# Kernel optimization log

Measured on AMD Instinct MI355X. Metric: run time of the kernel, lower is better.

The kernel has to match this reference:

```python
import jax, jax.numpy as jnp
import numpy as np

B = 4096
NUM_USERS = 100000
H_DIM = 128          # HIDDEN_DIM
IN_DIM = 128 + 8 + 32  # BOARD_FEAT_DIM + ACTION_BITS + USER_EMB_DIM


def _conv(x, w, b):
    # x: [B,C,H,W], w: [O,I,3,3] (torch OIHW), padding=1 -> SAME
    y = jax.lax.conv_general_dilated(
        x, w, window_strides=(1, 1), padding='SAME',
        dimension_numbers=('NCHW', 'OIHW', 'NCHW'))
    return y + b[None, :, None, None]


def _maxpool2(x):
    return jax.lax.reduce_window(x, -jnp.inf, jax.lax.max,
                                 (1, 1, 2, 2), (1, 1, 2, 2), 'VALID')


def setup_inputs() -> dict:
    key = jax.random.key(0)
    ks = jax.random.split(key, 24)
    f32 = jnp.float32

    def n(k, shape, s=0.05):
        return jax.random.normal(k, shape, dtype=f32) * s

    return {
        'board': jax.random.uniform(ks[0], (B, 1, 32, 32), dtype=f32),
        'h': jax.random.normal(ks[1], (1, B, H_DIM), dtype=f32),
        'action_token': jax.random.randint(ks[2], (B,), 0, 256, dtype=jnp.int32),
        'user_idx': jax.random.randint(ks[3], (B,), 0, NUM_USERS, dtype=jnp.int32),
        # SmallBoardCNN params
        'conv1_w': n(ks[4], (16, 1, 3, 3)), 'conv1_b': n(ks[5], (16,)),
        'conv2_w': n(ks[6], (32, 16, 3, 3)), 'conv2_b': n(ks[7], (32,)),
        'conv3_w': n(ks[8], (64, 32, 3, 3)), 'conv3_b': n(ks[9], (64,)),
        'conv4_w': n(ks[10], (128, 64, 3, 3)), 'conv4_b': n(ks[11], (128,)),
        'proj_w': n(ks[12], (128, 128)), 'proj_b': n(ks[13], (128,)),
        # user embedding
        'emb': n(ks[14], (NUM_USERS, 32), 1.0),
        # GRU params (torch layout: [3H, in], gate order r,z,n)
        'w_ih': n(ks[15], (3 * H_DIM, IN_DIM)), 'w_hh': n(ks[16], (3 * H_DIM, H_DIM)),
        'b_ih': n(ks[17], (3 * H_DIM,)), 'b_hh': n(ks[18], (3 * H_DIM,)),
        # head
        'head_w': n(ks[19], (6, H_DIM)), 'head_b': n(ks[20], (6,)),
    }


def reference(board, h, action_token, user_idx,
              conv1_w, conv1_b, conv2_w, conv2_b, conv3_w, conv3_b,
              conv4_w, conv4_b, proj_w, proj_b, emb,
              w_ih, w_hh, b_ih, b_hh, head_w, head_b):
    # SmallBoardCNN
    x = jax.nn.relu(_conv(board, conv1_w, conv1_b))
    x = jax.nn.relu(_conv(x, conv2_w, conv2_b))
    x = _maxpool2(x)                       # [B,32,16,16]
    x = jax.nn.relu(_conv(x, conv3_w, conv3_b))
    x = _maxpool2(x)                       # [B,64,8,8]
    x = jax.nn.relu(_conv(x, conv4_w, conv4_b))
    bf = x.mean(axis=(2, 3)) @ proj_w.T + proj_b   # AdaptiveAvgPool(1,1) + Linear -> [B,128]

    # int_to_8bits, batched
    abits = ((action_token[:, None] >> jnp.arange(8)) & 1).astype(jnp.float32)  # [B,8]
    uemb = emb[user_idx]                              # [B,32]
    xin = jnp.concatenate([bf, abits, uemb], axis=1)  # [B,168]

    # single GRU step (torch GRUCell math, gate order r,z,n)
    h0 = h[0]                                         # [B,128]
    gi = xin @ w_ih.T + b_ih                          # [B,384]
    gh = h0 @ w_hh.T + b_hh
    r = jax.nn.sigmoid(gi[:, :H_DIM] + gh[:, :H_DIM])
    z = jax.nn.sigmoid(gi[:, H_DIM:2 * H_DIM] + gh[:, H_DIM:2 * H_DIM])
    n_ = jnp.tanh(gi[:, 2 * H_DIM:] + r * gh[:, 2 * H_DIM:])
    h_new = (1.0 - z) * n_ + z * h0                   # [B,128]

    logits = h_new @ head_w.T + head_b                # [B,6]
    return logits, h_new[None]                        # h_new: [1,B,128]
```

## Files before the change

kernel.cpp:

```cpp
#include <hip/hip_runtime.h>
#include <hip/hip_bf16.h>

#define BATCH 4096

typedef __attribute__((ext_vector_type(8))) short short8;
typedef __attribute__((ext_vector_type(16))) float f32x16;

#define WB1_ELEM 0
#define WB2_ELEM 512
#define WB3_ELEM 5120
#define WB4_ELEM 23552
#define WB_TOTAL 97280

#define A1_OFF 2320
#define ZS1_OFF 19728
#define A2_OFF 19792
#define ZS2_OFF 36176
#define SMEM_F 36240
#define ZS3_REL 8192
#define MEANV_OFF 8320

static __device__ __forceinline__ unsigned pack2(float a, float b) {
    __hip_bfloat16 lo = __float2bfloat16(a), hi = __float2bfloat16(b);
    unsigned short ul = *(unsigned short*)&lo, uh = *(unsigned short*)&hi;
    return ((unsigned)uh << 16) | ul;
}

static __device__ __forceinline__ void store_bf16(void* p, float v) {
    __hip_bfloat16 b = __float2bfloat16(v);
    *(unsigned short*)p = *(unsigned short*)&b;
}

__global__ void prepack_weights(const float* __restrict__ w1,
                                const float* __restrict__ w2,
                                const float* __restrict__ w3,
                                const float* __restrict__ w4,
                                __hip_bfloat16* __restrict__ wb) {
    int g = blockIdx.x * 256 + threadIdx.x;
    if (g < 512) {
        int oc = g >> 4, k = g & 15;
        float v = (oc < 16 && k < 9) ? w1[oc * 9 + k] : 0.f;
        wb[g] = __float2bfloat16(v);
    } else if (g < WB3_ELEM) {
        int gg = g - WB2_ELEM;
        int oc = gg / 144, r = gg - oc * 144, tap = r >> 4, ic = r & 15;
        wb[g] = __float2bfloat16(w2[oc * 144 + ic * 9 + tap]);
    } else if (g < WB4_ELEM) {
        int gg = g - WB3_ELEM;
        int oc = gg / 288, r = gg - oc * 288, tap = r >> 5, ic = r & 31;
        wb[g] = __float2bfloat16(w3[oc * 288 + ic * 9 + tap]);
    } else if (g < WB_TOTAL) {
        int gg = g - WB4_ELEM;
        int oc = gg / 576, r = gg - oc * 576, tap = r >> 6, ic = r & 63;
        wb[g] = __float2bfloat16(w4[oc * 576 + ic * 9 + tap]);
    }
}

__global__ __launch_bounds__(256, 4) void cnn_fused_kernel(
    const float* __restrict__ board,
    const float* __restrict__ b1, const float* __restrict__ b2,
    const float* __restrict__ b3, const float* __restrict__ b4,
    const float* __restrict__ pw, const float* __restrict__ pb,
    const __hip_bfloat16* __restrict__ wb,
    float* __restrict__ bf_out)
{
    __shared__ alignas(16) char smem[SMEM_F];
    unsigned short* sbu = (unsigned short*)smem;
    char* a1b = smem + A1_OFF;
    char* a3b = smem;
    float* meanv = (float*)(smem + MEANV_OFF);

    const int t = threadIdx.x;
    const int img = blockIdx.x;
    const int w = t >> 6;
    const int l = t & 63;
    const int n = l & 31;
    const int h = l >> 5;

    const char* wb3 = (const char*)(wb + WB3_ELEM);
    const char* wb4 = (const char*)(wb + WB4_ELEM);

    {
        if (t < 132) {
            int i = t, row, col;
            if (i < 34)       { row = 0;  col = i; }
            else if (i < 68)  { row = 33; col = i - 34; }
            else if (i < 100) { row = i - 68 + 1;  col = 0; }
            else              { row = i - 100 + 1; col = 33; }
            sbu[row * 34 + col] = 0;
        }
        uint4 z; z.x = z.y = z.z = z.w = 0u;
        if (t >= 136 && t < 140) ((uint4*)(smem + ZS1_OFF))[t - 136] = z;
        else if (t >= 140 && t < 144) ((uint4*)(smem + ZS2_OFF))[t - 140] = z;
    }
    __syncthreads();

    {
        float4 v = ((const float4*)board)[img * 256 + t];
        const int p0 = t * 4;
        const int row = (p0 >> 5) + 1, col = (p0 & 31) + 1;
        unsigned short* d = sbu + row * 34 + col;
        __hip_bfloat16 x0 = __float2bfloat16(v.x), x1 = __float2bfloat16(v.y);
        __hip_bfloat16 x2 = __float2bfloat16(v.z), x3 = __float2bfloat16(v.w);
        d[0] = *(unsigned short*)&x0; d[1] = *(unsigned short*)&x1;
        d[2] = *(unsigned short*)&x2; d[3] = *(unsigned short*)&x3;
    }
    __syncthreads();

#pragma unroll 1
    for (int band = 0; band < 2; ++band) {
        const int base = band * 15;

        {
            const short8 A1 = *(const short8*)((const char*)wb + (n * 16 + h * 8) * 2);
            float b1s[8];
#pragma unroll
            for (int r = 0; r < 8; ++r) b1s[r] = b1[(r & 3) + 8 * (r >> 2) + 4 * h];
            const unsigned* sbw = (const unsigned*)smem;
#pragma unroll 1
            for (int yi = 0; yi < 5; ++yi) {
                if (yi == 4 && w != 0) break;
                const int yg = (yi < 4) ? (base + 4 * w + yi) : (base + 16);
                unsigned short c[3][3];
#pragma unroll
                for (int dy = 0; dy < 3; ++dy) {
                    const int sbase = (yg + dy) * 17 + (n >> 1);
                    const unsigned w0 = sbw[sbase], w1v = sbw[sbase + 1];
                    if (n & 1) {
                        c[dy][0] = (unsigned short)(w0 >> 16);
                        c[dy][1] = (unsigned short)(w1v & 0xffff);
                        c[dy][2] = (unsigned short)(w1v >> 16);
                    } else {
                        c[dy][0] = (unsigned short)(w0 & 0xffff);
                        c[dy][1] = (unsigned short)(w0 >> 16);
                        c[dy][2] = (unsigned short)(w1v & 0xffff);
                    }
                }
                short8 Bv;
                if (h == 0) {
                    Bv[0] = (short)c[0][0]; Bv[1] = (short)c[0][1]; Bv[2] = (short)c[0][2];
                    Bv[3] = (short)c[1][0]; Bv[4] = (short)c[1][1]; Bv[5] = (short)c[1][2];
                    Bv[6] = (short)c[2][0]; Bv[7] = (short)c[2][1];
                } else {
                    Bv = (short8)0;
                    Bv[0] = (short)c[2][2];
                }
                f32x16 acc = __builtin_amdgcn_mfma_f32_32x32x16_bf16(A1, Bv, (f32x16)0.0f, 0, 0, 0);
                float v8[8];
#pragma unroll
                for (int r = 0; r < 8; ++r) v8[r] = fmaxf(acc[r] + b1s[r], 0.f);
                const int key = ((n >> 2) & 1) << 4;
                char* dst = a1b + ((yg - base) * 32 + n) * 32;
                uint2 u0, u1;
                u0.x = pack2(v8[0], v8[1]); u0.y = pack2(v8[2], v8[3]);
                u1.x = pack2(v8[4], v8[5]); u1.y = pack2(v8[6], v8[7]);
                *(uint2*)(dst + ((h * 8) ^ key)) = u0;
                *(uint2*)(dst + ((h * 8 + 16) ^ key)) = u1;
            }
        }
        __syncthreads();

        {
            const char* wb2 = (const char*)(wb + WB2_ELEM);
            short8 Bw[9];
#pragma unroll
            for (int tp = 0; tp < 9; ++tp)
                Bw[tp] = *(const short8*)(wb2 + (n * 144 + tp * 16 + h * 8) * 2);
            const float biasv = b2[n];
            const int y_off = 2 * ((n >> 2) & 1) + ((n >> 1) & 1);
            const int x_off = 2 * ((n >> 3) & 3) + (n & 1);
            const int py_base = 8 * band + 2 * w;
            const int yb = 16 * band + 4 * w + y_off;

#pragma unroll 1
            for (int pxh = 0; pxh < 2; ++pxh) {
                const int x0 = 16 * pxh + x_off;
                f32x16 acc0 = (f32x16)0.0f, acc1 = (f32x16)0.0f;
#pragma unroll
                for (int tp = 0; tp < 9; ++tp) {
                    const int dy = tp / 3, dx = tp - 3 * dy;
                    const int lr = yb + dy - 1 - base;
                    const int c0 = x0 + dx - 1, c1 = x0 + 8 + dx - 1;
                    const bool okr = (unsigned)lr < 17u;
                    const int off0 = (okr && (unsigned)c0 < 32u)
                        ? (A1_OFF + (lr * 32 + c0) * 32 + ((h * 16) ^ (((c0 >> 2) & 1) << 4)))
                        : (ZS1_OFF + h * 16);
                    const int off1 = (okr && (unsigned)c1 < 32u)
                        ? (A1_OFF + (lr * 32 + c1) * 32 + ((h * 16) ^ (((c1 >> 2) & 1) << 4)))
                        : (ZS1_OFF + h * 16);
                    short8 A0 = *(const short8*)(smem + off0);
                    short8 A1v = *(const short8*)(smem + off1);
                    acc0 = __builtin_amdgcn_mfma_f32_32x32x16_bf16(A0, Bw[tp], acc0, 0, 0, 0);
                    acc1 = __builtin_amdgcn_mfma_f32_32x32x16_bf16(A1v, Bw[tp], acc1, 0, 0, 0);
                }
                const int py = py_base + h;
#pragma unroll
                for (int e = 0; e < 2; ++e) {
                    const f32x16 acc = e ? acc1 : acc0;
                    const int pxb = 2 * pxh + e;
#pragma unroll
                    for (int j = 0; j < 4; ++j) {
                        float v = fmaxf(fmaxf(acc[4 * j], acc[4 * j + 1]),
                                        fmaxf(acc[4 * j + 2], acc[4 * j + 3]));
                        v = fmaxf(v + biasv, 0.f);
                        const int px = 4 * pxb + j;
                        const int key = (py + 2 * px) & 3;
                        store_bf16(smem + A2_OFF + (py * 16 + px) * 64 +
                                   ((((n >> 3) ^ key) & 3) << 4) + ((n * 2) & 15), v);
                    }
                }
            }
        }
        __syncthreads();
    }

    {
        uint4 z; z.x = z.y = z.z = z.w = 0u;
        if (t < 8) ((uint4*)(a3b + ZS3_REL))[t] = z;
    }
    __syncthreads();

    {
        const int y_off = 2 * ((n >> 2) & 1) + ((n >> 1) & 1);
        const int x_off = 2 * ((n >> 3) & 3) + (n & 1);
        const int y_in = 4 * w + y_off;
        f32x16 acc00 = (f32x16)0.0f, acc01 = (f32x16)0.0f;
        f32x16 acc10 = (f32x16)0.0f, acc11 = (f32x16)0.0f;
#pragma unroll
        for (int step = 0; step < 18; ++step) {
            const int tp = step >> 1, kh = step & 1;
            const int dy = tp / 3, dx = tp - 3 * dy;
            short8 B0 = *(const short8*)(wb3 + ((n)      * 288 + tp * 32 + kh * 16 + h * 8) * 2);
            short8 B1 = *(const short8*)(wb3 + ((32 + n) * 288 + tp * 32 + kh * 16 + h * 8) * 2);
            const int row_u = y_in + dy - 1;
            const int col0 = x_off + dx - 1;
            const int col1 = col0 + 8;
            const int sbase = kh * 32 + h * 16;
            const bool okr = (unsigned)row_u < 16u;
            const int off0 = (okr && (unsigned)col0 < 16u)
                ? (A2_OFF + row_u * 1024 + col0 * 64 + (sbase ^ (((row_u + 2 * col0) & 3) << 4)))
                : (ZS2_OFF + sbase);
            const int off1 = (okr && (unsigned)col1 < 16u)
                ? (A2_OFF + row_u * 1024 + col1 * 64 + (sbase ^ (((row_u + 2 * col1) & 3) << 4)))
                : (ZS2_OFF + sbase);
            short8 A0 = *(const short8*)(smem + off0);
            short8 A1v = *(const short8*)(smem + off1);
            acc00 = __builtin_amdgcn_mfma_f32_32x32x16_bf16(A0, B0, acc00, 0, 0, 0);
            acc01 = __builtin_amdgcn_mfma_f32_32x32x16_bf16(A0, B1, acc01, 0, 0, 0);
            acc10 = __builtin_amdgcn_mfma_f32_32x32x16_bf16(A1v, B0, acc10, 0, 0, 0);
            acc11 = __builtin_amdgcn_mfma_f32_32x32x16_bf16(A1v, B1, acc11, 0, 0, 0);
        }
        const int py = 2 * w + h;
#pragma unroll
        for (int e = 0; e < 4; ++e) {
            const f32x16 acc = (e == 0) ? acc00 : (e == 1) ? acc01 : (e == 2) ? acc10 : acc11;
            const int pxb = e >> 1, ocb = e & 1;
            const float biasv = b3[32 * ocb + n];
#pragma unroll
            for (int j = 0; j < 4; ++j) {
                float v = fmaxf(fmaxf(acc[4 * j], acc[4 * j + 1]),
                                fmaxf(acc[4 * j + 2], acc[4 * j + 3]));
                v = fmaxf(v + biasv, 0.f);
                const int px = 4 * pxb + j;
                const int byte_in = ocb * 64 + n * 2;
                const int key3 = (py + 2 * px) & 7;
                store_bf16(a3b + (py * 8 + px) * 128 +
                           ((((byte_in >> 4) ^ key3) << 4) | (byte_in & 15)), v);
            }
        }
    }
    __syncthreads();

    {
        const int x4 = n & 7, y4 = (n >> 3) & 3;
        f32x16 aE0 = (f32x16)0.0f, aO0 = (f32x16)0.0f;
        f32x16 aE1 = (f32x16)0.0f, aO1 = (f32x16)0.0f;
#pragma unroll
        for (int dy = 0; dy < 3; ++dy)
#pragma unroll
            for (int dx = 0; dx < 3; ++dx) {
                const int row0 = y4 + dy - 1;
                const int col_u = x4 + dx - 1;
                const bool okc = (unsigned)col_u < 8u;
                const bool ok0 = okc && ((unsigned)row0 < 8u);
                const bool ok1 = okc && ((unsigned)(row0 + 4) < 8u);
#pragma unroll
                for (int kc = 0; kc < 4; ++kc) {
                    const int s4 = kc * 32 + h * 16;
                    const int off0 = ok0
                        ? ((row0 * 8 + col_u) * 128 + (s4 ^ (((row0 + 2 * col_u) & 7) << 4)))
                        : (ZS3_REL + s4);
                    const int off1 = ok1
                        ? (((row0 + 4) * 8 + col_u) * 128 + (s4 ^ (((row0 + 4 + 2 * col_u) & 7) << 4)))
                        : (ZS3_REL + s4);
                    short8 B = *(const short8*)(wb4 + ((32 * w + n) * 576 + (dy * 3 + dx) * 64 + kc * 16 + h * 8) * 2);
                    short8 A0 = *(const short8*)(a3b + off0);
                    short8 A1v = *(const short8*)(a3b + off1);
                    if (kc & 1) {
                        aO0 = __builtin_amdgcn_mfma_f32_32x32x16_bf16(A0, B, aO0, 0, 0, 0);
                        aO1 = __builtin_amdgcn_mfma_f32_32x32x16_bf16(A1v, B, aO1, 0, 0, 0);
                    } else {
                        aE0 = __builtin_amdgcn_mfma_f32_32x32x16_bf16(A0, B, aE0, 0, 0, 0);
                        aE1 = __builtin_amdgcn_mfma_f32_32x32x16_bf16(A1v, B, aE1, 0, 0, 0);
                    }
                }
            }
        const float biasv = b4[32 * w + n];
        float s = 0.f;
#pragma unroll
        for (int r = 0; r < 16; ++r) {
            s += fmaxf(aE0[r] + aO0[r] + biasv, 0.f);
            s += fmaxf(aE1[r] + aO1[r] + biasv, 0.f);
        }
        s += __shfl_xor(s, 32);
        if (l < 32) meanv[32 * w + l] = s * (1.f / 64.f);
    }
    __syncthreads();

    {
        const int o = t >> 1, kh = t & 1;
        const float* wrow = pw + o * 128 + kh * 64;
        const float* mv = meanv + kh * 64;
        float acc = 0.f;
        for (int k = 0; k < 64; ++k) acc = fmaf(mv[k], wrow[k], acc);
        acc += __shfl_xor(acc, 1);
        if (kh == 0) bf_out[img * 128 + o] = acc + pb[o];
    }
}

__global__ __launch_bounds__(384) void gru_kernel(
    const float* __restrict__ hin,
    const int* __restrict__ atok, const int* __restrict__ uidx,
    const float* __restrict__ emb,
    const float* __restrict__ w_ih, const float* __restrict__ w_hh,
    const float* __restrict__ b_ih, const float* __restrict__ b_hh,
    const float* __restrict__ head_w, const float* __restrict__ head_b,
    float* __restrict__ out)
{
    const int img0 = blockIdx.x * 8;
    const int t = threadIdx.x;
    __shared__ float xin_s[8][176];
    __shared__ float h0_s[8][128];
    __shared__ float gis[8][384];
    __shared__ float ghs[8][384];
    __shared__ float hn_s[8][128];
    const float* bf = out + BATCH * 6;

    for (int idx = t; idx < 8 * 176; idx += 384) {
        const int r = idx / 176, k = idx - r * 176;
        const int row = img0 + r;
        float v;
        if (k < 128)      v = bf[row * 128 + k];
        else if (k < 136) v = (float)((atok[row] >> (k - 128)) & 1);
        else if (k < 168) v = emb[uidx[row] * 32 + (k - 136)];
        else              v = 0.f;
        xin_s[r][k] = v;
    }
    for (int idx = t; idx < 8 * 128; idx += 384) {
        const int r = idx >> 7, k = idx & 127;
        h0_s[r][k] = hin[(img0 + r) * 128 + k];
    }
    __syncthreads();

    {
        const int o = t;
        float gi[8], gh[8];
        const float bi = b_ih[o], bh = b_hh[o];
#pragma unroll
        for (int r = 0; r < 8; ++r) { gi[r] = bi; gh[r] = bh; }
        const float* wi = w_ih + o * 168;
        const float* wh = w_hh + o * 128;
#pragma unroll 2
        for (int k = 0; k < 168; k += 4) {
            const float4 wv = *(const float4*)(wi + k);
#pragma unroll
            for (int r = 0; r < 8; ++r) {
                const float4 xv = *(const float4*)(&xin_s[r][k]);
                float a = fmaf(wv.x, xv.x, gi[r]);
                a = fmaf(wv.y, xv.y, a);
                a = fmaf(wv.z, xv.z, a);
                gi[r] = fmaf(wv.w, xv.w, a);
            }
        }
#pragma unroll 2
        for (int k = 0; k < 128; k += 4) {
            const float4 wv = *(const float4*)(wh + k);
#pragma unroll
            for (int r = 0; r < 8; ++r) {
                const float4 xv = *(const float4*)(&h0_s[r][k]);
                float a = fmaf(wv.x, xv.x, gh[r]);
                a = fmaf(wv.y, xv.y, a);
                a = fmaf(wv.z, xv.z, a);
                gh[r] = fmaf(wv.w, xv.w, a);
            }
        }
#pragma unroll
        for (int r = 0; r < 8; ++r) { gis[r][o] = gi[r]; ghs[r][o] = gh[r]; }
    }
    __syncthreads();

    if (t < 128) {
#pragma unroll
        for (int r = 0; r < 8; ++r) {
            const float rg = 1.f / (1.f + expf(-(gis[r][t] + ghs[r][t])));
            const float z  = 1.f / (1.f + expf(-(gis[r][128 + t] + ghs[r][128 + t])));
            const float nn = tanhf(gis[r][256 + t] + rg * ghs[r][256 + t]);
            const float hn = (1.f - z) * nn + z * h0_s[r][t];
            hn_s[r][t] = hn;
            out[BATCH * 6 + (img0 + r) * 128 + t] = hn;
        }
    }
    __syncthreads();

    if (t < 48) {
        const int r = t / 6, j = t - r * 6;
        float acc = head_b[j];
        const float* wrow = head_w + j * 128;
        for (int k = 0; k < 128; ++k) acc = fmaf(hn_s[r][k], wrow[k], acc);
        out[(img0 + r) * 6 + j] = acc;
    }
}

extern "C" void kernel_launch(void* const* d_in, const int* in_sizes, int n_in,
                              void* d_out, int out_size, void* d_ws, size_t ws_size,
                              hipStream_t stream) {
    const float* board = (const float*)d_in[0];
    const float* h     = (const float*)d_in[1];
    const int*   atok  = (const int*)d_in[2];
    const int*   uidx  = (const int*)d_in[3];
    const float* w1 = (const float*)d_in[4];
    const float* b1 = (const float*)d_in[5];
    const float* w2 = (const float*)d_in[6];
    const float* b2 = (const float*)d_in[7];
    const float* w3 = (const float*)d_in[8];
    const float* b3 = (const float*)d_in[9];
    const float* w4 = (const float*)d_in[10];
    const float* b4 = (const float*)d_in[11];
    const float* pw = (const float*)d_in[12];
    const float* pb = (const float*)d_in[13];
    const float* emb  = (const float*)d_in[14];
    const float* w_ih = (const float*)d_in[15];
    const float* w_hh = (const float*)d_in[16];
    const float* b_ih = (const float*)d_in[17];
    const float* b_hh = (const float*)d_in[18];
    const float* head_w = (const float*)d_in[19];
    const float* head_b = (const float*)d_in[20];
    float* out = (float*)d_out;
    __hip_bfloat16* wb = (__hip_bfloat16*)d_ws;

    float* bf = out + BATCH * 6;
    prepack_weights<<<(WB_TOTAL + 255) / 256, 256, 0, stream>>>(w1, w2, w3, w4, wb);
    cnn_fused_kernel<<<BATCH, 256, 0, stream>>>(board, b1, b2, b3, b4,
                                                pw, pb, wb, bf);
    gru_kernel<<<BATCH / 8, 384, 0, stream>>>(h, atok, uidx, emb, w_ih, w_hh,
                                              b_ih, b_hh, head_w, head_b, out);
}
```

Measured before the change: 191.8 us.

## Fuse GRU step and head into the per-image CNN kernel

Moves the GRU cell and output head into the CNN kernel so each block computes the features, gates and logits for its own image in shared memory. This drops the second kernel launch and the global write/read of the board features. In exchange, the GRU and head weights are streamed once per image instead of once per 8 images, which loses register reuse across rows and raises L2 traffic.

```diff
diff --git a/kernel.cpp b/kernel.cpp
--- a/kernel.cpp
+++ b/kernel.cpp
@@ -19,6 +19,11 @@
 #define SMEM_F 36240
 #define ZS3_REL 8192
 #define MEANV_OFF 8320
+#define GXIN_OFF 8832
+#define GH0_OFF 9536
+#define GGI_OFF 10048
+#define GGH_OFF 11584
+#define GHN_OFF 13120
 
 static __device__ __forceinline__ unsigned pack2(float a, float b) {
     __hip_bfloat16 lo = __float2bfloat16(a), hi = __float2bfloat16(b);
@@ -58,17 +63,28 @@
 
 __global__ __launch_bounds__(256, 4) void cnn_fused_kernel(
     const float* __restrict__ board,
+    const float* __restrict__ hin,
+    const int* __restrict__ atok, const int* __restrict__ uidx,
+    const float* __restrict__ emb,
     const float* __restrict__ b1, const float* __restrict__ b2,
     const float* __restrict__ b3, const float* __restrict__ b4,
     const float* __restrict__ pw, const float* __restrict__ pb,
+    const float* __restrict__ w_ih, const float* __restrict__ w_hh,
+    const float* __restrict__ b_ih, const float* __restrict__ b_hh,
+    const float* __restrict__ head_w, const float* __restrict__ head_b,
     const __hip_bfloat16* __restrict__ wb,
-    float* __restrict__ bf_out)
+    float* __restrict__ out)
 {
     __shared__ alignas(16) char smem[SMEM_F];
     unsigned short* sbu = (unsigned short*)smem;
     char* a1b = smem + A1_OFF;
     char* a3b = smem;
     float* meanv = (float*)(smem + MEANV_OFF);
+    float* xin = (float*)(smem + GXIN_OFF);
+    float* h0v = (float*)(smem + GH0_OFF);
+    float* gis = (float*)(smem + GGI_OFF);
+    float* ghs = (float*)(smem + GGH_OFF);
+    float* hnv = (float*)(smem + GHN_OFF);
 
     const int t = threadIdx.x;
     const int img = blockIdx.x;
@@ -217,6 +233,16 @@
     {
         uint4 z; z.x = z.y = z.z = z.w = 0u;
         if (t < 8) ((uint4*)(a3b + ZS3_REL))[t] = z;
+        else if (t >= 8 && t < 136) {
+            const int k = t - 8;
+            h0v[k] = hin[(size_t)img * 128 + k];
+        } else if (t < 144) {
+            const int k = t - 136 + 128;
+            xin[k] = (float)((atok[img] >> (k - 128)) & 1);
+        } else if (t < 176) {
+            const int k = t - 144 + 136;
+            xin[k] = emb[(size_t)uidx[img] * 32 + (k - 136)];
+        }
     }
     __syncthreads();
 
@@ -324,100 +350,61 @@
         float acc = 0.f;
         for (int k = 0; k < 64; ++k) acc = fmaf(mv[k], wrow[k], acc);
         acc += __shfl_xor(acc, 1);
-        if (kh == 0) bf_out[img * 128 + o] = acc + pb[o];
-    }
-}
-
-__global__ __launch_bounds__(384) void gru_kernel(
-    const float* __restrict__ hin,
-    const int* __restrict__ atok, const int* __restrict__ uidx,
-    const float* __restrict__ emb,
-    const float* __restrict__ w_ih, const float* __restrict__ w_hh,
-    const float* __restrict__ b_ih, const float* __restrict__ b_hh,
-    const float* __restrict__ head_w, const float* __restrict__ head_b,
-    float* __restrict__ out)
-{
-    const int img0 = blockIdx.x * 8;
-    const int t = threadIdx.x;
-    __shared__ float xin_s[8][176];
-    __shared__ float h0_s[8][128];
-    __shared__ float gis[8][384];
-    __shared__ float ghs[8][384];
-    __shared__ float hn_s[8][128];
-    const float* bf = out + BATCH * 6;
-
-    for (int idx = t; idx < 8 * 176; idx += 384) {
-        const int r = idx / 176, k = idx - r * 176;
-        const int row = img0 + r;
-        float v;
-        if (k < 128)      v = bf[row * 128 + k];
-        else if (k < 136) v = (float)((atok[row] >> (k - 128)) & 1);
-        else if (k < 168) v = emb[uidx[row] * 32 + (k - 136)];
-        else              v = 0.f;
-        xin_s[r][k] = v;
-    }
-    for (int idx = t; idx < 8 * 128; idx += 384) {
-        const int r = idx >> 7, k = idx & 127;
-        h0_s[r][k] = hin[(img0 + r) * 128 + k];
-    }
-    __syncthreads();
-
-    {
-        const int o = t;
-        float gi[8], gh[8];
-        const float bi = b_ih[o], bh = b_hh[o];
-#pragma unroll
-        for (int r = 0; r < 8; ++r) { gi[r] = bi; gh[r] = bh; }
-        const float* wi = w_ih + o * 168;
-        const float* wh = w_hh + o * 128;
+        if (kh == 0) xin[o] = acc + pb[o];
+    }
+    __syncthreads();
+
+    {
+#pragma unroll 1
+        for (int o = t; o < 384; o += 256) {
+            float gi = b_ih[o], gh = b_hh[o];
+            const float* wi = w_ih + o * 168;
+            const float* wh = w_hh + o * 128;
 #pragma unroll 2
-        for (int k = 0; k < 168; k += 4) {
-            const float4 wv = *(const float4*)(wi + k);
-#pragma unroll
-            for (int r = 0; r < 8; ++r) {
-                const float4 xv = *(const float4*)(&xin_s[r][k]);
-                float a = fmaf(wv.x, xv.x, gi[r]);
+            for (int k = 0; k < 168; k += 4) {
+                const float4 wv = *(const float4*)(wi + k);
+                const float4 xv = *(const float4*)(xin + k);
+                float a = fmaf(wv.x, xv.x, gi);
                 a = fmaf(wv.y, xv.y, a);
                 a = fmaf(wv.z, xv.z, a);
-                gi[r] = fmaf(wv.w, xv.w, a);
-            }
-        }
+                gi = fmaf(wv.w, xv.w, a);
+            }
 #pragma unroll 2
-        for (int k = 0; k < 128; k += 4) {
-            const float4 wv = *(const float4*)(wh + k);
-#pragma unroll
-            for (int r = 0; r < 8; ++r) {
-                const float4 xv = *(const float4*)(&h0_s[r][k]);
-                float a = fmaf(wv.x, xv.x, gh[r]);
+            for (int k = 0; k < 128; k += 4) {
+                const float4 wv = *(const float4*)(wh + k);
+                const float4 xv = *(const float4*)(h0v + k);
+                float a = fmaf(wv.x, xv.x, gh);
                 a = fmaf(wv.y, xv.y, a);
                 a = fmaf(wv.z, xv.z, a);
-                gh[r] = fmaf(wv.w, xv.w, a);
-            }
-        }
-#pragma unroll
-        for (int r = 0; r < 8; ++r) { gis[r][o] = gi[r]; ghs[r][o] = gh[r]; }
+                gh = fmaf(wv.w, xv.w, a);
+            }
+            gis[o] = gi;
+            ghs[o] = gh;
+        }
     }
     __syncthreads();
 
     if (t < 128) {
-#pragma unroll
-        for (int r = 0; r < 8; ++r) {
-            const float rg = 1.f / (1.f + expf(-(gis[r][t] + ghs[r][t])));
-            const float z  = 1.f / (1.f + expf(-(gis[r][128 + t] + ghs[r][128 + t])));
-            const float nn = tanhf(gis[r][256 + t] + rg * ghs[r][256 + t]);
-            const float hn = (1.f - z) * nn + z * h0_s[r][t];
-            hn_s[r][t] = hn;
-            out[BATCH * 6 + (img0 + r) * 128 + t] = hn;
-        }
-    }
-    __syncthreads();
-
-    if (t < 48) {
-        const int r = t / 6, j = t - r * 6;
-        float acc = head_b[j];
-        const float* wrow = head_w + j * 128;
-        for (int k = 0; k < 128; ++k) acc = fmaf(hn_s[r][k], wrow[k], acc);
-        out[(img0 + r) * 6 + j] = acc;
+        const float rg = 1.f / (1.f + expf(-(gis[t] + ghs[t])));
+        const float zz = 1.f / (1.f + expf(-(gis[128 + t] + ghs[128 + t])));
+        const float nn = tanhf(gis[256 + t] + rg * ghs[256 + t]);
+        const float hn = (1.f - zz) * nn + zz * h0v[t];
+        hnv[t] = hn;
+        out[BATCH * 6 + (size_t)img * 128 + t] = hn;
+    }
+    __syncthreads();
+
+    if (t < 192) {
+        const int j = t >> 5, lane = t & 31;
+        const float4 wv = *(const float4*)(head_w + j * 128 + lane * 4);
+        const float4 hv = *(const float4*)(hnv + lane * 4);
+        float s = wv.x * hv.x + wv.y * hv.y + wv.z * hv.z + wv.w * hv.w;
+        s += __shfl_xor(s, 16);
+        s += __shfl_xor(s, 8);
+        s += __shfl_xor(s, 4);
+        s += __shfl_xor(s, 2);
+        s += __shfl_xor(s, 1);
+        if (lane == 0) out[(size_t)img * 6 + j] = s + head_b[j];
     }
 }
 
@@ -448,10 +435,9 @@
     float* out = (float*)d_out;
     __hip_bfloat16* wb = (__hip_bfloat16*)d_ws;
 
-    float* bf = out + BATCH * 6;
     prepack_weights<<<(WB_TOTAL + 255) / 256, 256, 0, stream>>>(w1, w2, w3, w4, wb);
-    cnn_fused_kernel<<<BATCH, 256, 0, stream>>>(board, b1, b2, b3, b4,
-                                                pw, pb, wb, bf);
-    gru_kernel<<<BATCH / 8, 384, 0, stream>>>(h, atok, uidx, emb, w_ih, w_hh,
-                                              b_ih, b_hh, head_w, head_b, out);
+    cnn_fused_kernel<<<BATCH, 256, 0, stream>>>(board, h, atok, uidx, emb,
+                                                b1, b2, b3, b4, pw, pb,
+                                                w_ih, w_hh, b_ih, b_hh,
+                                                head_w, head_b, wb, out);
 }
```

Result: slower. 349.8 us (+82.4%).
